# Kernel tuning notes

Hardware: AMD Instinct MI355X
Metric: run time of the kernel (lower is better)

The kernel has to match this reference:

```python
import jax, jax.numpy as jnp
import numpy as np

B, S, D = 8, 1024, 256


def _linear_params(key, d):
    k1, k2 = jax.random.split(key)
    lim = 1.0 / np.sqrt(d)
    W = jax.random.uniform(k1, (d, d), jnp.float32, -lim, lim)
    b = jax.random.uniform(k2, (d,), jnp.float32, -lim, lim)
    return W, b


def setup_inputs() -> dict:
    key = jax.random.key(0)
    ks = jax.random.split(key, 7)
    x = jax.random.normal(ks[0], (B, S, D), jnp.float32)
    Wq, bq = _linear_params(ks[1], D)
    Wk, bk = _linear_params(ks[2], D)
    Wv, bv = _linear_params(ks[3], D)
    Wf, bf = _linear_params(ks[4], D)
    Wi, bi = _linear_params(ks[5], D)
    Wo, bo = _linear_params(ks[6], D)
    return {"x": x, "Wq": Wq, "bq": bq, "Wk": Wk, "bk": bk, "Wv": Wv, "bv": bv,
            "Wf": Wf, "bf": bf, "Wi": Wi, "bi": bi, "Wo": Wo, "bo": bo}


def reference(x, Wq, bq, Wk, bk, Wv, bv, Wf, bf, Wi, bi, Wo, bo):
    # Projections (torch Linear stores W as [out, in])
    q = x @ Wq.T + bq
    k = x @ Wk.T + bk
    v = x @ Wq.T + bq  # faithful to source: forward uses self.W_q(x) for v (W_v unused)
    f = jax.nn.sigmoid(x @ Wf.T + bf)  # forget gate, sigmoid
    i = jnp.exp(x @ Wi.T + bi)         # input gate, exp

    # time-major xs: each (S, B, D)
    xs = tuple(jnp.swapaxes(a, 0, 1) for a in (f, i, k, v, q))
    C0 = jnp.zeros((x.shape[0], x.shape[2], x.shape[2]), x.dtype)  # matrix memory [B,D,D]
    n0 = jnp.zeros((x.shape[0], x.shape[2]), x.dtype)              # normalizer [B,D]

    def step(carry, t):
        C, n = carry
        ft, it, kt, vt, qt = t
        # C_t = f_t * C_{t-1} + i_t * v_t k_t^T  (gates broadcast over key dim)
        C = ft[:, :, None] * C + it[:, :, None] * (vt[:, :, None] * kt[:, None, :])
        n = ft * n + it * kt
        num = jnp.einsum('bik,bk->bi', C, qt)
        den = jnp.maximum(jnp.abs(jnp.einsum('bk,bk->b', n, qt)), 1.0)[:, None]
        return (C, n), num / den

    _, h = jax.lax.scan(step, (C0, n0), xs)
    h = jnp.swapaxes(h, 0, 1)  # (B, S, D)
    return h @ Wo.T + bo
```

## Files before the change

kernel.cpp:

```cpp
#include <hip/hip_runtime.h>
#include <math.h>

namespace {

constexpr int Bn = 8;
constexpr int Sn = 1024;
constexpr int Dn = 256;
constexpr int Mn = Bn * Sn;
constexpr int L  = 32;
constexpr int NSEG = Sn / L;

typedef __attribute__((ext_vector_type(8))) short short8;
typedef __attribute__((ext_vector_type(4))) float f32x4;

__device__ float g_den[Bn * Sn];

__device__ __forceinline__ float sigmoidf_(float x) {
    return 1.0f / (1.0f + __expf(-x));
}

__device__ __forceinline__ unsigned short f2bf(float x) {
    unsigned int u = __float_as_uint(x);
    return (unsigned short)((u + 0x7FFF + ((u >> 16) & 1)) >> 16);
}
__device__ __forceinline__ float bf2f(unsigned short h) {
    return __uint_as_float(((unsigned int)h) << 16);
}

__global__ __launch_bounds__(256) void split_xw(
    const float* __restrict__ X,
    const float* __restrict__ Wq, const float* __restrict__ Wk,
    const float* __restrict__ Wf, const float* __restrict__ Wi,
    unsigned short* __restrict__ Xh, unsigned short* __restrict__ Xl,
    unsigned short* __restrict__ Wh, unsigned short* __restrict__ Wl)
{
    const int i = blockIdx.x * 256 + threadIdx.x;
    const float4* src;
    unsigned short* dh;
    unsigned short* dl;
    size_t off;
    if (i < 524288) {
        src = (const float4*)X + i;
        dh = Xh; dl = Xl;
        off = (size_t)i * 4;
    } else {
        const int j = i - 524288;
        const int w = j >> 14;
        const int r = j & 16383;
        const float* Wp = (w == 0) ? Wq : (w == 1) ? Wk : (w == 2) ? Wf : Wi;
        src = (const float4*)Wp + r;
        dh = Wh; dl = Wl;
        off = ((size_t)w << 16) + (size_t)r * 4;
    }
    const float4 v = *src;
    ushort4 h, l;
    h.x = f2bf(v.x); l.x = f2bf(v.x - bf2f(h.x));
    h.y = f2bf(v.y); l.y = f2bf(v.y - bf2f(h.y));
    h.z = f2bf(v.z); l.z = f2bf(v.z - bf2f(h.z));
    h.w = f2bf(v.w); l.w = f2bf(v.w - bf2f(h.w));
    *(ushort4*)(dh + off) = h;
    *(ushort4*)(dl + off) = l;
}

__global__ __launch_bounds__(256) void split_pn(
    const float* __restrict__ Pn, const float* __restrict__ Wo,
    unsigned short* __restrict__ Ph, unsigned short* __restrict__ Pl,
    unsigned short* __restrict__ Woh, unsigned short* __restrict__ Wol)
{
    const int i = blockIdx.x * 256 + threadIdx.x;
    float4 v;
    unsigned short* dh;
    unsigned short* dl;
    size_t off;
    if (i < 524288) {
        const float invd = 1.0f / fmaxf(fabsf(g_den[i >> 6]), 1.0f);
        v = ((const float4*)Pn)[i];
        v.x *= invd; v.y *= invd; v.z *= invd; v.w *= invd;
        dh = Ph; dl = Pl;
        off = (size_t)i * 4;
    } else {
        const int j = i - 524288;
        v = ((const float4*)Wo)[j];
        dh = Woh; dl = Wol;
        off = (size_t)j * 4;
    }
    ushort4 h, l;
    h.x = f2bf(v.x); l.x = f2bf(v.x - bf2f(h.x));
    h.y = f2bf(v.y); l.y = f2bf(v.y - bf2f(h.y));
    h.z = f2bf(v.z); l.z = f2bf(v.z - bf2f(h.z));
    h.w = f2bf(v.w); l.w = f2bf(v.w - bf2f(h.w));
    *(ushort4*)(dh + off) = h;
    *(ushort4*)(dl + off) = l;
}

__global__ __launch_bounds__(256) void proj_gemm2(
    const unsigned short* __restrict__ Xh, const unsigned short* __restrict__ Xl,
    const unsigned short* __restrict__ Wh, const unsigned short* __restrict__ Wl,
    const float* __restrict__ b0, const float* __restrict__ b1,
    const float* __restrict__ b2, const float* __restrict__ b3,
    float* __restrict__ Y0, float* __restrict__ Y1,
    float* __restrict__ Y2, float* __restrict__ Y3)
{
    const int tid = threadIdx.x;
    const int mb  = blockIdx.x * 128;
    const int nbg = blockIdx.y;
    const int widx = nbg >> 1;
    const int ro   = (nbg & 1) * 128;

    const float* bsel = (widx == 0) ? b0 : (widx == 1) ? b1 : (widx == 2) ? b2 : b3;
    float*       Ysel = (widx == 0) ? Y0 : (widx == 1) ? Y1 : (widx == 2) ? Y2 : Y3;

    const int lane = tid & 63;
    const int wv   = tid >> 6;
    const int wm   = (wv >> 1) * 64;
    const int wn   = (wv & 1) * 64;
    const int quad = lane >> 4;
    const int l16  = lane & 15;

    size_t arow[4], brow[4];
    #pragma unroll
    for (int mt = 0; mt < 4; ++mt)
        arow[mt] = (size_t)(mb + wm + mt * 16 + l16) * Dn + quad * 8;
    #pragma unroll
    for (int nt = 0; nt < 4; ++nt)
        brow[nt] = (size_t)(nbg * 128 + wn + nt * 16 + l16) * Dn + quad * 8;

    f32x4 acc[4][4];
    #pragma unroll
    for (int mt = 0; mt < 4; ++mt)
        #pragma unroll
        for (int nt = 0; nt < 4; ++nt)
            acc[mt][nt] = (f32x4){0.f, 0.f, 0.f, 0.f};

    for (int k0 = 0; k0 < Dn; k0 += 32) {
        short8 afh[4], afl[4], bfh[4], bfl[4];
        #pragma unroll
        for (int mt = 0; mt < 4; ++mt) {
            afh[mt] = *(const short8*)(Xh + arow[mt] + k0);
            afl[mt] = *(const short8*)(Xl + arow[mt] + k0);
        }
        #pragma unroll
        for (int nt = 0; nt < 4; ++nt) {
            bfh[nt] = *(const short8*)(Wh + brow[nt] + k0);
            bfl[nt] = *(const short8*)(Wl + brow[nt] + k0);
        }
        #pragma unroll
        for (int nt = 0; nt < 4; ++nt) {
            #pragma unroll
            for (int mt = 0; mt < 4; ++mt) {
                acc[mt][nt] = __builtin_amdgcn_mfma_f32_16x16x32_bf16(
                    afh[mt], bfh[nt], acc[mt][nt], 0, 0, 0);
                acc[mt][nt] = __builtin_amdgcn_mfma_f32_16x16x32_bf16(
                    afh[mt], bfl[nt], acc[mt][nt], 0, 0, 0);
                acc[mt][nt] = __builtin_amdgcn_mfma_f32_16x16x32_bf16(
                    afl[mt], bfh[nt], acc[mt][nt], 0, 0, 0);
            }
        }
    }

    #pragma unroll
    for (int nt = 0; nt < 4; ++nt) {
        const int col = ro + wn + nt * 16 + l16;
        const float bv = bsel[col];
        #pragma unroll
        for (int mt = 0; mt < 4; ++mt) {
            const int rowb = mb + wm + mt * 16 + quad * 4;
            #pragma unroll
            for (int r = 0; r < 4; ++r) {
                float v = acc[mt][nt][r] + bv;
                if (widx == 2)      v = sigmoidf_(v);
                else if (widx == 3) v = __expf(v);
                Ysel[(size_t)(rowb + r) * Dn + col] = v;
            }
        }
    }
}

__global__ __launch_bounds__(256) void out_gemm2(
    const unsigned short* __restrict__ Ph, const unsigned short* __restrict__ Pl,
    const unsigned short* __restrict__ Woh, const unsigned short* __restrict__ Wol,
    const float* __restrict__ bias, float* __restrict__ Y)
{
    __shared__ unsigned short Ahs[64][40];
    __shared__ unsigned short Als[64][40];
    __shared__ unsigned short Bhs[64][40];
    __shared__ unsigned short Bls[64][40];

    const int tid = threadIdx.x;
    const int mb  = blockIdx.x * 64;
    const int nb  = blockIdx.y * 64;

    const int lane = tid & 63;
    const int wv   = tid >> 6;
    const int wm   = (wv >> 1) * 32;
    const int wn   = (wv & 1) * 32;
    const int quad = lane >> 4;
    const int l16  = lane & 15;
    const int srow = tid >> 2;
    const int skq  = (tid & 3) * 8;

    const size_t abase = (size_t)(mb + srow) * Dn + skq;
    const size_t bbase = (size_t)(nb + srow) * Dn + skq;

    f32x4 acc[2][2];
    #pragma unroll
    for (int mt = 0; mt < 2; ++mt)
        #pragma unroll
        for (int nt = 0; nt < 2; ++nt)
            acc[mt][nt] = (f32x4){0.f, 0.f, 0.f, 0.f};

    short8 pah, pal, pbh, pbl;
    pah = *(const short8*)(Ph  + abase);
    pal = *(const short8*)(Pl  + abase);
    pbh = *(const short8*)(Woh + bbase);
    pbl = *(const short8*)(Wol + bbase);

    for (int k0 = 0; k0 < Dn; k0 += 32) {
        __syncthreads();
        *(short8*)&Ahs[srow][skq] = pah;
        *(short8*)&Als[srow][skq] = pal;
        *(short8*)&Bhs[srow][skq] = pbh;
        *(short8*)&Bls[srow][skq] = pbl;
        __syncthreads();

        if (k0 + 32 < Dn) {
            const size_t ka = abase + k0 + 32;
            const size_t kb = bbase + k0 + 32;
            pah = *(const short8*)(Ph  + ka);
            pal = *(const short8*)(Pl  + ka);
            pbh = *(const short8*)(Woh + kb);
            pbl = *(const short8*)(Wol + kb);
        }

        short8 afh[2], afl[2];
        #pragma unroll
        for (int mt = 0; mt < 2; ++mt) {
            const int row = wm + mt * 16 + l16;
            afh[mt] = *(const short8*)&Ahs[row][quad * 8];
            afl[mt] = *(const short8*)&Als[row][quad * 8];
        }
        #pragma unroll
        for (int nt = 0; nt < 2; ++nt) {
            const int row = wn + nt * 16 + l16;
            const short8 bfh = *(const short8*)&Bhs[row][quad * 8];
            const short8 bfl = *(const short8*)&Bls[row][quad * 8];
            #pragma unroll
            for (int mt = 0; mt < 2; ++mt) {
                acc[mt][nt] = __builtin_amdgcn_mfma_f32_16x16x32_bf16(
                    afh[mt], bfh, acc[mt][nt], 0, 0, 0);
                acc[mt][nt] = __builtin_amdgcn_mfma_f32_16x16x32_bf16(
                    afh[mt], bfl, acc[mt][nt], 0, 0, 0);
                acc[mt][nt] = __builtin_amdgcn_mfma_f32_16x16x32_bf16(
                    afl[mt], bfh, acc[mt][nt], 0, 0, 0);
            }
        }
    }

    #pragma unroll
    for (int nt = 0; nt < 2; ++nt) {
        const int col = nb + wn + nt * 16 + l16;
        const float bv = bias[col];
        #pragma unroll
        for (int mt = 0; mt < 2; ++mt) {
            const int rowb = mb + wm + mt * 16 + quad * 4;
            #pragma unroll
            for (int r = 0; r < 4; ++r) {
                Y[(size_t)(rowb + r) * Dn + col] = acc[mt][nt][r] + bv;
            }
        }
    }
}

__global__ __launch_bounds__(512) void prep(
    const float* __restrict__ Pf, const float* __restrict__ Pi,
    const float* __restrict__ Pk, const float* __restrict__ Pq,
    float* __restrict__ Gc, float* __restrict__ Vt, float* __restrict__ Nt,
    float* __restrict__ Aend, float* __restrict__ un, float* __restrict__ Ssm)
{
    __shared__ float Ks[L][260];
    __shared__ float Qs[L][260];

    const int m = blockIdx.x;
    const int b = blockIdx.y;
    const int tid = threadIdx.x;
    const size_t qb = (size_t)b * Sn * Dn + (size_t)m * L * Dn;

    if (tid < L) g_den[b * Sn + m * L + tid] = 0.0f;

    #pragma unroll
    for (int p = 0; p < 4; ++p) {
        const int lin = p * 512 + tid;
        const int row = lin >> 6;
        const int c4  = (lin & 63) * 4;
        *(float4*)&Ks[row][c4] = *(const float4*)(Pk + qb + (size_t)row * Dn + c4);
    }
    #pragma unroll
    for (int p = 0; p < 4; ++p) {
        const int lin = p * 512 + tid;
        const int row = lin >> 6;
        const int c4  = (lin & 63) * 4;
        *(float4*)&Qs[row][c4] = *(const float4*)(Pq + qb + (size_t)row * Dn + c4);
    }
    __syncthreads();

    if (tid < 256) {
        const int r = tid;
        const size_t base = qb + r;
        float G = 1.0f, Nacc = 0.0f;
        for (int tb = 0; tb < L; tb += 8) {
            float fv[8], iv[8];
            #pragma unroll
            for (int u = 0; u < 8; ++u) {
                fv[u] = Pf[base + (size_t)(tb + u) * Dn];
                iv[u] = Pi[base + (size_t)(tb + u) * Dn];
            }
            #pragma unroll
            for (int u = 0; u < 8; ++u) {
                const int t = tb + u;
                const size_t off = base + (size_t)t * Dn;
                const float kv = Ks[t][r];
                const float vv = Qs[t][r];
                G *= fv[u];
                const float rG = 1.0f / G;
                Gc[off] = G;
                Vt[off] = iv[u] * vv * rG;
                Nacc = fmaf(iv[u] * kv, rG, Nacc);
                Nt[off] = Nacc;
            }
        }
        const size_t s = ((size_t)b * NSEG + m) * Dn + r;
        Aend[s] = G;
        un[s]   = G * Nacc;
    } else {
        const int t2  = tid - 256;
        const int tau = t2 >> 3;
        const int sb0 = t2 & 7;

        float a0 = 0.f, a1 = 0.f, a2 = 0.f, a3 = 0.f;
        #pragma unroll 4
        for (int c = 0; c < Dn; c += 4) {
            const float4 q4 = *(const float4*)&Qs[tau][c];
            const float4 k0 = *(const float4*)&Ks[sb0     ][c];
            const float4 k1 = *(const float4*)&Ks[sb0 +  8][c];
            const float4 k2 = *(const float4*)&Ks[sb0 + 16][c];
            const float4 k3 = *(const float4*)&Ks[sb0 + 24][c];
            a0 += q4.x*k0.x + q4.y*k0.y + q4.z*k0.z + q4.w*k0.w;
            a1 += q4.x*k1.x + q4.y*k1.y + q4.z*k1.z + q4.w*k1.w;
            a2 += q4.x*k2.x + q4.y*k2.y + q4.z*k2.z + q4.w*k2.w;
            a3 += q4.x*k3.x + q4.y*k3.y + q4.z*k3.z + q4.w*k3.w;
        }
        float* outp = Ssm + ((size_t)b * NSEG + m) * L * L + (size_t)tau * L;
        outp[sb0     ] = (sb0      <= tau) ? a0 : 0.0f;
        outp[sb0 +  8] = (sb0 +  8 <= tau) ? a1 : 0.0f;
        outp[sb0 + 16] = (sb0 + 16 <= tau) ? a2 : 0.0f;
        outp[sb0 + 24] = (sb0 + 24 <= tau) ? a3 : 0.0f;
    }
}

__global__ __launch_bounds__(256) void ut_gemm(
    const float* __restrict__ Pk, const float* __restrict__ Vt,
    const float* __restrict__ Aend, float* __restrict__ UT)
{
    __shared__ float As[L][68];
    __shared__ float Bs[L][68];

    const int bm   = blockIdx.x;
    const int tile = blockIdx.y;
    const int cb   = (tile >> 2) * 64;
    const int rb   = (tile & 3) * 64;
    const int b    = bm >> 5;
    const int m    = bm & 31;
    const size_t kb = (size_t)b * Sn * Dn + (size_t)m * L * Dn;
    const int tid = threadIdx.x;

    #pragma unroll
    for (int n = 0; n < 8; ++n) {
        const int e  = n * 256 + tid;
        const int sg = e >> 6;
        const int cc = e & 63;
        As[sg][cc] = Pk[kb + (size_t)sg * Dn + cb + cc];
        Bs[sg][cc] = Vt[kb + (size_t)sg * Dn + rb + cc];
    }
    __syncthreads();

    const int tx = tid & 15;
    const int ty = tid >> 4;
    float acc[4][4];
    #pragma unroll
    for (int i = 0; i < 4; ++i)
        #pragma unroll
        for (int j = 0; j < 4; ++j) acc[i][j] = 0.0f;

    #pragma unroll
    for (int sg = 0; sg < L; ++sg) {
        const float4 a4 = *(const float4*)&As[sg][ty * 4];
        const float4 b4 = *(const float4*)&Bs[sg][tx * 4];
        const float aa[4] = {a4.x, a4.y, a4.z, a4.w};
        const float bb[4] = {b4.x, b4.y, b4.z, b4.w};
        #pragma unroll
        for (int i = 0; i < 4; ++i)
            #pragma unroll
            for (int j = 0; j < 4; ++j)
                acc[i][j] = fmaf(aa[i], bb[j], acc[i][j]);
    }

    const float4 g4 = *(const float4*)(Aend + (size_t)bm * Dn + rb + tx * 4);
    float* ub = UT + (size_t)bm * Dn * Dn;
    #pragma unroll
    for (int i = 0; i < 4; ++i) {
        float4 o;
        o.x = acc[i][0] * g4.x; o.y = acc[i][1] * g4.y;
        o.z = acc[i][2] * g4.z; o.w = acc[i][3] * g4.w;
        *(float4*)(ub + (size_t)(cb + ty * 4 + i) * Dn + rb + tx * 4) = o;
    }
}

__global__ __launch_bounds__(256) void compose(
    const float* __restrict__ UT, const float* __restrict__ Aend,
    const float* __restrict__ un,
    float* __restrict__ CinT, float* __restrict__ nin)
{
    const int gx = blockIdx.x;
    const int b  = blockIdx.y;
    const int tid = threadIdx.x;

    if (gx == 32) {
        const int r = tid;
        float acc = 0.0f;
        for (int m = 0; m < NSEG; ++m) {
            const size_t s = ((size_t)b * NSEG + m) * Dn + r;
            nin[s] = acc;
            acc = fmaf(Aend[s], acc, un[s]);
        }
        return;
    }

    const int id = gx * 256 + tid;
    const int c  = id >> 5;
    const int r8 = (id & 31) * 8;

    float4 acc0 = make_float4(0.f, 0.f, 0.f, 0.f);
    float4 acc1 = make_float4(0.f, 0.f, 0.f, 0.f);
    for (int m = 0; m < NSEG; ++m) {
        const size_t bm  = (size_t)b * NSEG + m;
        const size_t idx = bm * Dn * Dn + (size_t)c * Dn + r8;
        const float4 a40 = *(const float4*)(Aend + bm * Dn + r8);
        const float4 a41 = *(const float4*)(Aend + bm * Dn + r8 + 4);
        const float4 u40 = *(const float4*)(UT + idx);
        const float4 u41 = *(const float4*)(UT + idx + 4);
        *(float4*)(CinT + idx)     = acc0;
        *(float4*)(CinT + idx + 4) = acc1;
        acc0.x = fmaf(a40.x, acc0.x, u40.x);
        acc0.y = fmaf(a40.y, acc0.y, u40.y);
        acc0.z = fmaf(a40.z, acc0.z, u40.z);
        acc0.w = fmaf(a40.w, acc0.w, u40.w);
        acc1.x = fmaf(a41.x, acc1.x, u41.x);
        acc1.y = fmaf(a41.y, acc1.y, u41.y);
        acc1.z = fmaf(a41.z, acc1.z, u41.z);
        acc1.w = fmaf(a41.w, acc1.w, u41.w);
    }
}

__global__ __launch_bounds__(256) void num_gemm(
    const float* __restrict__ Pq, const float* __restrict__ Vt,
    const float* __restrict__ Gc, const float* __restrict__ Ssm,
    const float* __restrict__ CinT, const float* __restrict__ Nt,
    const float* __restrict__ nin, float* __restrict__ Pnum)
{
    __shared__ float Sld[L][33];
    __shared__ float Qld[L][257];

    const int rb = blockIdx.x * 128;
    const int m  = blockIdx.y;
    const int b  = blockIdx.z;
    const size_t qb = (size_t)b * Sn * Dn + (size_t)m * L * Dn;
    const size_t ub = ((size_t)b * NSEG + m) * Dn * Dn;
    const size_t sb = ((size_t)b * NSEG + m) * L * L;
    const int tid = threadIdx.x;

    #pragma unroll
    for (int n = 0; n < 4; ++n) {
        const int e = n * 256 + tid;
        Sld[e >> 5][e & 31] = Ssm[sb + e];
    }
    #pragma unroll
    for (int n = 0; n < L; ++n)
        Qld[n][tid] = Pq[qb + (size_t)n * Dn + tid];
    __syncthreads();

    const int tx = tid & 31;
    const int ty = tid >> 5;
    const int r4 = rb + tx * 4;
    const int t4 = ty * 4;

    float4 acc[4];
    #pragma unroll
    for (int i = 0; i < 4; ++i) acc[i] = make_float4(0.f, 0.f, 0.f, 0.f);

    #pragma unroll 4
    for (int sg = 0; sg < L; ++sg) {
        const float4 v4 = *(const float4*)(Vt + qb + (size_t)sg * Dn + r4);
        #pragma unroll
        for (int i = 0; i < 4; ++i) {
            const float s = Sld[t4 + i][sg];
            acc[i].x = fmaf(s, v4.x, acc[i].x);
            acc[i].y = fmaf(s, v4.y, acc[i].y);
            acc[i].z = fmaf(s, v4.z, acc[i].z);
            acc[i].w = fmaf(s, v4.w, acc[i].w);
        }
    }

    #pragma unroll 8
    for (int c = 0; c < Dn; ++c) {
        const float4 ct = *(const float4*)(CinT + ub + (size_t)c * Dn + r4);
        #pragma unroll
        for (int i = 0; i < 4; ++i) {
            const float q = Qld[t4 + i][c];
            acc[i].x = fmaf(q, ct.x, acc[i].x);
            acc[i].y = fmaf(q, ct.y, acc[i].y);
            acc[i].z = fmaf(q, ct.z, acc[i].z);
            acc[i].w = fmaf(q, ct.w, acc[i].w);
        }
    }

    const float4 i4 = *(const float4*)(nin + ((size_t)b * NSEG + m) * Dn + r4);
    float dp[4];
    #pragma unroll
    for (int i = 0; i < 4; ++i) {
        const size_t off = qb + (size_t)(t4 + i) * Dn + r4;
        const float4 g4 = *(const float4*)(Gc + off);
        const float4 q4 = *(const float4*)(Pq + off);
        const float4 n4 = *(const float4*)(Nt + off);
        float4 o;
        o.x = acc[i].x * g4.x; o.y = acc[i].y * g4.y;
        o.z = acc[i].z * g4.z; o.w = acc[i].w * g4.w;
        *(float4*)(Pnum + off) = o;
        dp[i] = q4.x * g4.x * (i4.x + n4.x)
              + q4.y * g4.y * (i4.y + n4.y)
              + q4.z * g4.z * (i4.z + n4.z)
              + q4.w * g4.w * (i4.w + n4.w);
    }

    #pragma unroll
    for (int s = 1; s < 32; s <<= 1) {
        #pragma unroll
        for (int i = 0; i < 4; ++i)
            dp[i] += __shfl_xor(dp[i], s, 64);
    }
    if (tx == 0) {
        #pragma unroll
        for (int i = 0; i < 4; ++i)
            atomicAdd(&g_den[b * Sn + m * L + t4 + i], dp[i]);
    }
}

}

extern "C" void kernel_launch(void* const* d_in, const int* in_sizes, int n_in,
                              void* d_out, int out_size, void* d_ws, size_t ws_size,
                              hipStream_t stream)
{
    const float* x  = (const float*)d_in[0];
    const float* Wq = (const float*)d_in[1];  const float* bq = (const float*)d_in[2];
    const float* Wk = (const float*)d_in[3];  const float* bk = (const float*)d_in[4];
    const float* Wf = (const float*)d_in[7];  const float* bf = (const float*)d_in[8];
    const float* Wi = (const float*)d_in[9];  const float* bi = (const float*)d_in[10];
    const float* Wo = (const float*)d_in[11]; const float* bo = (const float*)d_in[12];
    float* out = (float*)d_out;

    float* ws = (float*)d_ws;
    const size_t sz = (size_t)Mn * Dn;
    float* Pq = ws;
    float* Pk = ws + sz;
    float* Pf = ws + 2 * sz;
    float* Pi = ws + 3 * sz;
    float* Pn = ws + 4 * sz;
    float* Gc = ws + 5 * sz;
    float* Vt = ws + 6 * sz;
    float* Nt = ws + 7 * sz;
    float* UT   = ws + 8 * sz;
    float* CinT = ws + 16 * sz;
    float* Ssm  = ws + 24 * sz;
    float* Aend = Ssm + (size_t)Bn * NSEG * L * L;
    float* un   = Aend + (size_t)Bn * NSEG * Dn;
    float* nin  = un   + (size_t)Bn * NSEG * Dn;

    unsigned short* Xh = (unsigned short*)UT;
    unsigned short* Xl = Xh + sz;
    unsigned short* Wh = Xl + sz;
    unsigned short* Wl = Wh + (size_t)1024 * Dn;
    unsigned short* Ph  = (unsigned short*)UT;
    unsigned short* Pl  = Ph + sz;
    unsigned short* Woh = (unsigned short*)Ssm;
    unsigned short* Wol = Woh + (size_t)Dn * Dn;

    split_xw<<<dim3(2304), 256, 0, stream>>>(x, Wq, Wk, Wf, Wi, Xh, Xl, Wh, Wl);

    proj_gemm2<<<dim3(Mn / 128, 8), 256, 0, stream>>>(
        Xh, Xl, Wh, Wl, bq, bk, bf, bi, Pq, Pk, Pf, Pi);

    prep<<<dim3(NSEG, Bn), 512, 0, stream>>>(
        Pf, Pi, Pk, Pq, Gc, Vt, Nt, Aend, un, Ssm);

    ut_gemm<<<dim3(Bn * NSEG, 16), 256, 0, stream>>>(Pk, Vt, Aend, UT);

    compose<<<dim3(33, Bn), 256, 0, stream>>>(UT, Aend, un, CinT, nin);

    num_gemm<<<dim3(2, NSEG, Bn), 256, 0, stream>>>(
        Pq, Vt, Gc, Ssm, CinT, Nt, nin, Pn);

    split_pn<<<dim3(2112), 256, 0, stream>>>(Pn, Wo, Ph, Pl, Woh, Wol);

    out_gemm2<<<dim3(Mn / 64, Dn / 64), 256, 0, stream>>>(
        Ph, Pl, Woh, Wol, bo, out);
}
```

Measured before the change: 215.4 us.

## Stage projection GEMM tiles through double-buffered LDS with direct global-to-LDS loads

The projection GEMM used to load its A and B fragments directly from global memory into registers for every MFMA tile. Now each 32-wide k-slice of the hi/lo bf16 tiles is copied into shared memory with global_load_lds, using two buffers so the next slice loads while the current one is computed. This is meant to cut redundant global traffic across waves and hide load latency. It costs 64 KB of LDS per block, which may reduce occupancy, and adds a barrier per k-step. There is no explicit wait on the async LDS loads before the barrier, so correctness relies on the compiler inserting vmcnt waits.

```diff
diff --git a/kernel.cpp b/kernel.cpp
--- a/kernel.cpp
+++ b/kernel.cpp
@@ -25,6 +25,13 @@
 }
 __device__ __forceinline__ float bf2f(unsigned short h) {
     return __uint_as_float(((unsigned int)h) << 16);
+}
+
+__device__ __forceinline__ void gload_lds16(const void* g, void* l) {
+    __builtin_amdgcn_global_load_lds(
+        (__attribute__((address_space(1))) void*)g,
+        (__attribute__((address_space(3))) void*)l,
+        16, 0, 0);
 }
 
 __global__ __launch_bounds__(256) void split_xw(
@@ -93,7 +100,7 @@
     *(ushort4*)(dl + off) = l;
 }
 
-__global__ __launch_bounds__(256) void proj_gemm2(
+__global__ __launch_bounds__(256) void proj_gemm3(
     const unsigned short* __restrict__ Xh, const unsigned short* __restrict__ Xl,
     const unsigned short* __restrict__ Wh, const unsigned short* __restrict__ Wl,
     const float* __restrict__ b0, const float* __restrict__ b1,
@@ -101,6 +108,11 @@
     float* __restrict__ Y0, float* __restrict__ Y1,
     float* __restrict__ Y2, float* __restrict__ Y3)
 {
+    __shared__ unsigned short Ahs[2][128][32];
+    __shared__ unsigned short Als[2][128][32];
+    __shared__ unsigned short Bhs[2][128][32];
+    __shared__ unsigned short Bls[2][128][32];
+
     const int tid = threadIdx.x;
     const int mb  = blockIdx.x * 128;
     const int nbg = blockIdx.y;
@@ -117,13 +129,12 @@
     const int quad = lane >> 4;
     const int l16  = lane & 15;
 
-    size_t arow[4], brow[4];
-    #pragma unroll
-    for (int mt = 0; mt < 4; ++mt)
-        arow[mt] = (size_t)(mb + wm + mt * 16 + l16) * Dn + quad * 8;
-    #pragma unroll
-    for (int nt = 0; nt < 4; ++nt)
-        brow[nt] = (size_t)(nbg * 128 + wn + nt * 16 + l16) * Dn + quad * 8;
+    const int sr = wv * 32 + (lane >> 2);
+    const int sc = (lane & 3) * 8;
+
+    const size_t agb = (size_t)(mb + sr) * Dn + sc;
+    const size_t bgb = (size_t)(nbg * 128 + sr) * Dn + sc;
+    const size_t rstep = (size_t)16 * Dn;
 
     f32x4 acc[4][4];
     #pragma unroll
@@ -132,31 +143,51 @@
         for (int nt = 0; nt < 4; ++nt)
             acc[mt][nt] = (f32x4){0.f, 0.f, 0.f, 0.f};
 
+#define STAGE_PROJ(buf, k0)                                                  \
+    do {                                                                     \
+        gload_lds16(Xh + agb + (k0),         &Ahs[buf][sr][sc]);             \
+        gload_lds16(Xh + agb + rstep + (k0), &Ahs[buf][sr + 16][sc]);        \
+        gload_lds16(Xl + agb + (k0),         &Als[buf][sr][sc]);             \
+        gload_lds16(Xl + agb + rstep + (k0), &Als[buf][sr + 16][sc]);        \
+        gload_lds16(Wh + bgb + (k0),         &Bhs[buf][sr][sc]);             \
+        gload_lds16(Wh + bgb + rstep + (k0), &Bhs[buf][sr + 16][sc]);        \
+        gload_lds16(Wl + bgb + (k0),         &Bls[buf][sr][sc]);             \
+        gload_lds16(Wl + bgb + rstep + (k0), &Bls[buf][sr + 16][sc]);        \
+    } while (0)
+
+    STAGE_PROJ(0, 0);
+    __syncthreads();
+
+    int cur = 0;
     for (int k0 = 0; k0 < Dn; k0 += 32) {
-        short8 afh[4], afl[4], bfh[4], bfl[4];
+        if (k0 + 32 < Dn) STAGE_PROJ(cur ^ 1, k0 + 32);
+
+        short8 afh[4], afl[4];
         #pragma unroll
         for (int mt = 0; mt < 4; ++mt) {
-            afh[mt] = *(const short8*)(Xh + arow[mt] + k0);
-            afl[mt] = *(const short8*)(Xl + arow[mt] + k0);
+            const int row = wm + mt * 16 + l16;
+            afh[mt] = *(const short8*)&Ahs[cur][row][quad * 8];
+            afl[mt] = *(const short8*)&Als[cur][row][quad * 8];
         }
         #pragma unroll
         for (int nt = 0; nt < 4; ++nt) {
-            bfh[nt] = *(const short8*)(Wh + brow[nt] + k0);
-            bfl[nt] = *(const short8*)(Wl + brow[nt] + k0);
-        }
-        #pragma unroll
-        for (int nt = 0; nt < 4; ++nt) {
+            const int row = wn + nt * 16 + l16;
+            const short8 bfh = *(const short8*)&Bhs[cur][row][quad * 8];
+            const short8 bfl = *(const short8*)&Bls[cur][row][quad * 8];
             #pragma unroll
             for (int mt = 0; mt < 4; ++mt) {
                 acc[mt][nt] = __builtin_amdgcn_mfma_f32_16x16x32_bf16(
-                    afh[mt], bfh[nt], acc[mt][nt], 0, 0, 0);
+                    afh[mt], bfh, acc[mt][nt], 0, 0, 0);
                 acc[mt][nt] = __builtin_amdgcn_mfma_f32_16x16x32_bf16(
-                    afh[mt], bfl[nt], acc[mt][nt], 0, 0, 0);
+                    afh[mt], bfl, acc[mt][nt], 0, 0, 0);
                 acc[mt][nt] = __builtin_amdgcn_mfma_f32_16x16x32_bf16(
-                    afl[mt], bfh[nt], acc[mt][nt], 0, 0, 0);
+                    afl[mt], bfh, acc[mt][nt], 0, 0, 0);
             }
         }
-    }
+        __syncthreads();
+        cur ^= 1;
+    }
+#undef STAGE_PROJ
 
     #pragma unroll
     for (int nt = 0; nt < 4; ++nt) {
@@ -596,7 +627,7 @@
 
     split_xw<<<dim3(2304), 256, 0, stream>>>(x, Wq, Wk, Wf, Wi, Xh, Xl, Wh, Wl);
 
-    proj_gemm2<<<dim3(Mn / 128, 8), 256, 0, stream>>>(
+    proj_gemm3<<<dim3(Mn / 128, 8), 256, 0, stream>>>(
         Xh, Xl, Wh, Wl, bq, bk, bf, bi, Pq, Pk, Pf, Pi);
 
     prep<<<dim3(NSEG, Bn), 512, 0, stream>>>(
```

Result: faster. 209.0 us (-3.0%).
